# Optimization experiments

Measured on AMD Instinct MI355X. Metric: run time of the kernel, lower is better.

## Reference

```python
import jax, jax.numpy as jnp
import numpy as np

TAU = 1.0  # gumbel_temperature
K = 8      # number of template rows (hard-coded for SCAN)


def _forward(decodings, type_emb, w_sem, b_sem, gumbel, target_types, spans):
    B, N, M, V = decodings.shape
    # --- per-example template logits: decoder_sem[span-2][type-9](type_embedding[type]) ---
    emb = type_emb[target_types]                  # [B,H]
    w = w_sem[target_types - 9]                   # [B, K*(N+1), H]
    b = b_sem[target_types - 9]                   # [B, K*(N+1)]
    logits = (jnp.einsum('bkh,bh->bk', w, emb) + b).reshape(B, K, N + 1)
    # ragged span: only positions 0..span are valid (original views to (K, s+1))
    pos = jnp.arange(N + 1)
    valid_pos = pos[None, None, :] <= spans[:, None, None]
    logits = jnp.where(valid_pos, logits, jnp.float32(-1e30))
    logp = jax.nn.log_softmax(logits, axis=-1)
    # hard gumbel-softmax with straight-through estimator (F.gumbel_softmax hard=True)
    y_soft = jax.nn.softmax((logp + gumbel) / TAU, axis=-1)
    y_hard = jax.nn.one_hot(jnp.argmax(y_soft, -1), N + 1, dtype=y_soft.dtype)
    dt = y_hard + y_soft - jax.lax.stop_gradient(y_soft)     # [B,K,N+1]
    # special start template for target type 20: row 0 selects child 1, rest select pad (0)
    start = jax.nn.one_hot(jnp.where(jnp.arange(K) == 0, 1, 0), N + 1, dtype=dt.dtype)
    dt = jnp.where((target_types == 20)[:, None, None], start[None], dt)
    # --- apply_decoder_template ---
    pad = jnp.zeros((M, V), decodings.dtype).at[:, 0].set(1.0)  # pad vector, token 0
    choices = jnp.concatenate(
        [jnp.broadcast_to(pad[None, None], (B, 1, M, V)), decodings], axis=1)  # [B,N+1,M,V]
    out = jnp.einsum('bkn,bnmv->bkmv', dt, choices)              # [B,K,M,V]
    # per-template effective length: last position whose argmax token != 0
    out_idx = jnp.argmax(out, axis=-1)                           # [B,K,M]
    jpos = jnp.arange(M)
    lens = jnp.max(jnp.where(out_idx != 0, jpos + 1, 0), axis=-1).astype(jnp.int32)  # [B,K]
    # sequential packing of the K template outputs, clipped at M (scan over K=8)
    def step(idx, l):
        eff = jnp.minimum(l, M - idx)
        return idx + eff, (idx, eff)
    _, (offsets, effs) = jax.lax.scan(step, jnp.zeros(B, jnp.int32), lens.T)
    offsets, effs = offsets.T, effs.T                            # [B,K]
    dest = offsets[:, :, None] + jpos[None, None, :]             # [B,K,M]
    valid = jpos[None, None, :] < effs[:, :, None]
    dest = jnp.where(valid, dest, M)                             # dump invalid writes to row M
    bidx = jnp.arange(B)[:, None, None]
    vals = jnp.where(valid[..., None], out, 0.0)
    result = jnp.zeros((B, M + 1, V), decodings.dtype)
    result = result.at[bidx, dest].set(vals)
    return result[:, :M]                                         # new_d: [B,M,V]


def setup_inputs() -> dict:
    key = jax.random.key(0)
    ks = jax.random.split(key, 6)
    B, N, M, V, H, T = 256, 16, 128, 64, 128, 24
    decodings = jax.random.normal(ks[0], (B, N, M, V), jnp.float32)
    type_emb = jax.random.normal(ks[1], (T, H), jnp.float32)
    w_sem = jax.random.normal(ks[2], (T - 9, K * (N + 1), H), jnp.float32) * 0.05
    b_sem = jnp.zeros((T - 9, K * (N + 1)), jnp.float32)
    u = jax.random.uniform(ks[3], (B, K, N + 1), jnp.float32, 1e-6, 1.0 - 1e-6)
    gumbel = -jnp.log(-jnp.log(u))
    target_types = jax.random.randint(ks[4], (B,), 9, T)  # valid decoder_sem type range
    spans = jnp.full((B,), N, dtype=jnp.int32)
    return {"decodings": decodings, "type_emb": type_emb, "w_sem": w_sem,
            "b_sem": b_sem, "gumbel": gumbel, "target_types": target_types,
            "spans": spans}


def reference(decodings, type_emb, w_sem, b_sem, gumbel, target_types, spans):
    return _forward(decodings, type_emb, w_sem, b_sem, gumbel, target_types, spans)
```

## Files before the change

kernel.cpp:

```cpp
#include <hip/hip_runtime.h>

constexpr int Bn  = 256;
constexpr int Nn  = 16;
constexpr int Mn  = 128;
constexpr int Vn  = 64;
constexpr int Hn  = 128;
constexpr int Kn  = 8;
constexpr int NP1 = 17;
constexpr int KN  = Kn * NP1;

__global__ __launch_bounds__(256) void fused_template_pack(
    const float* __restrict__ dec,
    const float* __restrict__ type_emb,
    const float* __restrict__ w_sem,
    const float* __restrict__ b_sem,
    const float* __restrict__ gumbel,
    const int*   __restrict__ ttypes,
    const int*   __restrict__ spans,
    float*       __restrict__ out)
{
    const int b    = blockIdx.x;
    const int tid  = threadIdx.x;
    const int lane = tid & 63;
    const int wave = tid >> 6;

    __shared__ float s_scores[KN];
    __shared__ int   s_sel[Kn];
    __shared__ int   s_len[Kn];
    __shared__ int   s_off[Kn];
    __shared__ int   s_eff[Kn];
    __shared__ int   s_total;

    const int t    = ttypes[b];
    const int span = spans[b];

    if (t != 20) {
        if (tid < KN) {
            const int n = tid % NP1;
            float score = -1e30f;
            if (n <= span) {
                const float4* wrow = (const float4*)(w_sem + ((size_t)(t - 9) * KN + tid) * Hn);
                const float4* erow = (const float4*)(type_emb + (size_t)t * Hn);
                float acc = 0.f;
                #pragma unroll
                for (int i = 0; i < Hn / 4; ++i) {
                    float4 wv = wrow[i];
                    float4 ev = erow[i];
                    acc += wv.x * ev.x + wv.y * ev.y + wv.z * ev.z + wv.w * ev.w;
                }
                score = acc + b_sem[(t - 9) * KN + tid] + gumbel[(size_t)b * KN + tid];
            }
            s_scores[tid] = score;
        }
        __syncthreads();
        if (tid < Kn) {
            int best = 0;
            float bv = s_scores[tid * NP1];
            #pragma unroll
            for (int n = 1; n < NP1; ++n) {
                float v = s_scores[tid * NP1 + n];
                if (v > bv) { bv = v; best = n; }
            }
            s_sel[tid] = best;
        }
    } else {
        if (tid < Kn) s_sel[tid] = (tid == 0) ? 1 : 0;
    }
    __syncthreads();

    for (int k = wave; k < Kn; k += 4) {
        const int s = s_sel[k];
        int local = 0;
        if (s > 0) {
            const float* row = dec + (((size_t)b * Nn + (s - 1)) * Mn) * Vn;
            #pragma unroll
            for (int half = 0; half < 2; ++half) {
                const int m = lane + half * 64;
                const float4* p = (const float4*)(row + (size_t)m * Vn);
                float bv = -__builtin_inff();
                int bidx = 0;
                #pragma unroll
                for (int j = 0; j < Vn / 4; ++j) {
                    float4 v4 = p[j];
                    if (v4.x > bv) { bv = v4.x; bidx = 4 * j + 0; }
                    if (v4.y > bv) { bv = v4.y; bidx = 4 * j + 1; }
                    if (v4.z > bv) { bv = v4.z; bidx = 4 * j + 2; }
                    if (v4.w > bv) { bv = v4.w; bidx = 4 * j + 3; }
                }
                if (bidx != 0) local = max(local, m + 1);
            }
        }
        #pragma unroll
        for (int d = 32; d > 0; d >>= 1)
            local = max(local, __shfl_xor(local, d, 64));
        if (lane == 0) s_len[k] = local;
    }
    __syncthreads();

    if (tid == 0) {
        int idx = 0;
        #pragma unroll
        for (int k = 0; k < Kn; ++k) {
            const int eff = min(s_len[k], Mn - idx);
            s_off[k] = idx;
            s_eff[k] = eff;
            idx += eff;
        }
        s_total = idx;
    }
    __syncthreads();

    float4* outb = (float4*)(out + (size_t)b * Mn * Vn);
    for (int k = 0; k < Kn; ++k) {
        const int eff = s_eff[k];
        if (eff == 0) continue;
        const float4* src =
            (const float4*)(dec + (((size_t)b * Nn + (s_sel[k] - 1)) * Mn) * Vn);
        float4* dst = outb + (size_t)s_off[k] * (Vn / 4);
        const int cnt = eff * (Vn / 4);
        for (int i = tid; i < cnt; i += 256) dst[i] = src[i];
    }

    const int total = s_total;
    const int zcnt  = (Mn - total) * (Vn / 4);
    float4* zdst = outb + (size_t)total * (Vn / 4);
    const float4 zero = make_float4(0.f, 0.f, 0.f, 0.f);
    for (int i = tid; i < zcnt; i += 256) zdst[i] = zero;
}

extern "C" void kernel_launch(void* const* d_in, const int* in_sizes, int n_in,
                              void* d_out, int out_size, void* d_ws, size_t ws_size,
                              hipStream_t stream) {
    const float* dec      = (const float*)d_in[0];
    const float* type_emb = (const float*)d_in[1];
    const float* w_sem    = (const float*)d_in[2];
    const float* b_sem    = (const float*)d_in[3];
    const float* gumbel   = (const float*)d_in[4];
    const int*   ttypes   = (const int*)d_in[5];
    const int*   spans    = (const int*)d_in[6];
    float* out = (float*)d_out;

    fused_template_pack<<<Bn, 256, 0, stream>>>(
        dec, type_emb, w_sem, b_sem, gumbel, ttypes, spans, out);
}
```

Baseline: 192.8 us.

## Scan template rows backward with wave-wide argmax and early exit, 512 threads

The length computation now scans each selected child's rows from the last position backward. The 64 lanes cooperatively compute each row's argmax via shuffles and stop at the first row whose argmax is non-zero, instead of reading all 128 rows. The block size doubles to 512 so each of the 8 templates gets its own wave. With random inputs the argmax is rarely 0, so the scan usually ends after one row, removing most of the read traffic. The cost is a serial per-row dependency chain of shuffles when early exit does not happen.

```diff
diff --git a/kernel.cpp b/kernel.cpp
--- a/kernel.cpp
+++ b/kernel.cpp
@@ -9,7 +9,7 @@
 constexpr int NP1 = 17;
 constexpr int KN  = Kn * NP1;
 
-__global__ __launch_bounds__(256) void fused_template_pack(
+__global__ __launch_bounds__(512) void fused_template_pack(
     const float* __restrict__ dec,
     const float* __restrict__ type_emb,
     const float* __restrict__ w_sem,
@@ -68,32 +68,24 @@
     }
     __syncthreads();
 
-    for (int k = wave; k < Kn; k += 4) {
-        const int s = s_sel[k];
-        int local = 0;
+    if (wave < Kn) {
+        const int s = s_sel[wave];
+        int len = 0;
         if (s > 0) {
             const float* row = dec + (((size_t)b * Nn + (s - 1)) * Mn) * Vn;
-            #pragma unroll
-            for (int half = 0; half < 2; ++half) {
-                const int m = lane + half * 64;
-                const float4* p = (const float4*)(row + (size_t)m * Vn);
-                float bv = -__builtin_inff();
-                int bidx = 0;
+            for (int m = Mn - 1; m >= 0; --m) {
+                float bv = row[(size_t)m * Vn + lane];
+                int   bi = lane;
                 #pragma unroll
-                for (int j = 0; j < Vn / 4; ++j) {
-                    float4 v4 = p[j];
-                    if (v4.x > bv) { bv = v4.x; bidx = 4 * j + 0; }
-                    if (v4.y > bv) { bv = v4.y; bidx = 4 * j + 1; }
-                    if (v4.z > bv) { bv = v4.z; bidx = 4 * j + 2; }
-                    if (v4.w > bv) { bv = v4.w; bidx = 4 * j + 3; }
+                for (int d = 1; d < 64; d <<= 1) {
+                    float ov = __shfl_xor(bv, d, 64);
+                    int   oi = __shfl_xor(bi, d, 64);
+                    if (ov > bv || (ov == bv && oi < bi)) { bv = ov; bi = oi; }
                 }
-                if (bidx != 0) local = max(local, m + 1);
+                if (bi != 0) { len = m + 1; break; }
             }
         }
-        #pragma unroll
-        for (int d = 32; d > 0; d >>= 1)
-            local = max(local, __shfl_xor(local, d, 64));
-        if (lane == 0) s_len[k] = local;
+        if (lane == 0) s_len[wave] = len;
     }
     __syncthreads();
 
@@ -118,14 +110,14 @@
             (const float4*)(dec + (((size_t)b * Nn + (s_sel[k] - 1)) * Mn) * Vn);
         float4* dst = outb + (size_t)s_off[k] * (Vn / 4);
         const int cnt = eff * (Vn / 4);
-        for (int i = tid; i < cnt; i += 256) dst[i] = src[i];
+        for (int i = tid; i < cnt; i += 512) dst[i] = src[i];
     }
 
     const int total = s_total;
     const int zcnt  = (Mn - total) * (Vn / 4);
     float4* zdst = outb + (size_t)total * (Vn / 4);
     const float4 zero = make_float4(0.f, 0.f, 0.f, 0.f);
-    for (int i = tid; i < zcnt; i += 256) zdst[i] = zero;
+    for (int i = tid; i < zcnt; i += 512) zdst[i] = zero;
 }
 
 extern "C" void kernel_launch(void* const* d_in, const int* in_sizes, int n_in,
@@ -140,6 +132,6 @@
     const int*   spans    = (const int*)d_in[6];
     float* out = (float*)d_out;
 
-    fused_template_pack<<<Bn, 256, 0, stream>>>(
+    fused_template_pack<<<Bn, 512, 0, stream>>>(
         dec, type_emb, w_sem, b_sem, gumbel, ttypes, spans, out);
 }
```

New measurement: 181.1 us. 6.1% less time.
